# Kernel tuning notes

Hardware: AMD Instinct MI355X
Metric: run time of the kernel (lower is better)

Reference implementation:

```python
import jax, jax.numpy as jnp
import numpy as np

N_GROUPS = 32
N_HEADS = 8
EPS = 1e-5


def group_norm(x, w, b):
    # x: [B, C, T]; GroupNorm32 computes in fp32 then casts back
    B, C, T = x.shape
    xf = x.astype(jnp.float32).reshape(B, N_GROUPS, (C // N_GROUPS) * T)
    mean = xf.mean(axis=-1, keepdims=True)
    var = xf.var(axis=-1, keepdims=True)
    xn = ((xf - mean) * jax.lax.rsqrt(var + EPS)).reshape(B, C, T)
    return (xn * w[None, :, None] + b[None, :, None]).astype(x.dtype)


def attention_block(x, norm_w, norm_b, qkv_w, qkv_b, proj_w, proj_b):
    B, C = x.shape[0], x.shape[1]
    spatial = x.shape[2:]
    xr = x.reshape(B, C, -1)  # [B, C, T]
    T = xr.shape[-1]
    h = group_norm(xr, norm_w, norm_b)
    # 1x1 Conv1d == per-position matmul: [B, 3C, T]
    qkv = jnp.einsum('oc,bct->bot', qkv_w, h) + qkv_b[None, :, None]
    ch = C // N_HEADS  # per-head channels
    q, k, v = jnp.split(qkv, 3, axis=1)
    q = q.reshape(B * N_HEADS, ch, T)
    k = k.reshape(B * N_HEADS, ch, T)
    v = v.reshape(B * N_HEADS, ch, T)
    scale = 1.0 / np.sqrt(ch)
    w = jnp.einsum('bct,bcs->bts', q * scale, k)  # [B*H, T, T]
    w = jax.nn.softmax(w.astype(jnp.float32), axis=-1).astype(w.dtype)
    a = jnp.einsum('bts,bcs->bct', w, v).reshape(B, C, T)
    a = jnp.einsum('oc,bct->bot', proj_w, a) + proj_b[None, :, None]
    return (xr + a).reshape(B, C, *spatial)


def setup_inputs() -> dict:
    key = jax.random.key(0)
    ks = jax.random.split(key, 6)
    B, C, H, W = 16, 512, 32, 32
    return {
        'x': jax.random.normal(ks[0], (B, C, H, W), jnp.float32),
        'norm_w': jnp.ones((C,), jnp.float32),
        'norm_b': jnp.zeros((C,), jnp.float32),
        'qkv_w': jax.random.normal(ks[1], (3 * C, C), jnp.float32) * (1.0 / np.sqrt(C)),
        'qkv_b': jax.random.normal(ks[2], (3 * C,), jnp.float32) * 0.02,
        'proj_w': jax.random.normal(ks[3], (C, C), jnp.float32) * (1.0 / np.sqrt(C)),
        'proj_b': jax.random.normal(ks[4], (C,), jnp.float32) * 0.02,
    }


def reference(x, norm_w, norm_b, qkv_w, qkv_b, proj_w, proj_b):
    return attention_block(x, norm_w, norm_b, qkv_w, qkv_b, proj_w, proj_b)
```

## Files before the change

kernel.cpp:

```cpp
#include <hip/hip_runtime.h>
#include <hip/hip_bf16.h>

#define B_ 16
#define C_ 512
#define T_ 1024
#define G_ 32
#define CPG 16
#define NH 8
#define CH 64
#define EPS 1e-5f

typedef __bf16 bf16x8 __attribute__((ext_vector_type(8)));
typedef __bf16 bf16x4 __attribute__((ext_vector_type(4)));
typedef float f32x4 __attribute__((ext_vector_type(4)));
typedef float f32x16 __attribute__((ext_vector_type(16)));
typedef int i32x4 __attribute__((ext_vector_type(4)));

__device__ __forceinline__ void gload16(const __bf16* g, const __bf16* l) {
    __builtin_amdgcn_global_load_lds(
        (const __attribute__((address_space(1))) unsigned int*)(unsigned long long)(uintptr_t)g,
        (__attribute__((address_space(3))) unsigned int*)(unsigned int)(uintptr_t)l,
        16, 0, 0);
}

__global__ __launch_bounds__(256) void convw_kernel(const float* __restrict__ qw,
                                                    const float* __restrict__ pw,
                                                    __bf16* __restrict__ wqb,
                                                    __bf16* __restrict__ wpb) {
    int idx = (blockIdx.x * 256 + threadIdx.x) * 8;
    const float* src;
    __bf16* dst;
    if (idx < 1536 * 512) { src = qw + idx; dst = wqb + idx; }
    else { src = pw + (idx - 1536 * 512); dst = wpb + (idx - 1536 * 512); }
    float4 a = *(const float4*)src, b = *(const float4*)(src + 4);
    bf16x8 t;
    t[0] = (__bf16)a.x; t[1] = (__bf16)a.y; t[2] = (__bf16)a.z; t[3] = (__bf16)a.w;
    t[4] = (__bf16)b.x; t[5] = (__bf16)b.y; t[6] = (__bf16)b.z; t[7] = (__bf16)b.w;
    *(bf16x8*)dst = t;
}

__global__ __launch_bounds__(256) void gn_kernel(const float* __restrict__ x,
                                                 const float* __restrict__ w,
                                                 const float* __restrict__ bvec,
                                                 __bf16* __restrict__ h_t) {
    const int blk = blockIdx.x;
    const int bb = blk >> 5;
    const int g  = blk & 31;
    const size_t base = ((size_t)bb * C_ + (size_t)g * CPG) * T_;
    const float4* xp = (const float4*)(x + base);
    float4 vals[16];
    float s = 0.f, sq = 0.f;
#pragma unroll
    for (int i = 0; i < 16; ++i) {
        float4 v = xp[threadIdx.x + i * 256];
        vals[i] = v;
        s  += v.x + v.y + v.z + v.w;
        sq += v.x * v.x + v.y * v.y + v.z * v.z + v.w * v.w;
    }
#pragma unroll
    for (int off = 32; off > 0; off >>= 1) {
        s  += __shfl_down(s, off);
        sq += __shfl_down(sq, off);
    }
    __shared__ float red[2][4];
    const int lane = threadIdx.x & 63, wid = threadIdx.x >> 6;
    if (lane == 0) { red[0][wid] = s; red[1][wid] = sq; }
    __syncthreads();
    s  = red[0][0] + red[0][1] + red[0][2] + red[0][3];
    sq = red[1][0] + red[1][1] + red[1][2] + red[1][3];
    const float mean = s * (1.f / 16384.f);
    const float var  = sq * (1.f / 16384.f) - mean * mean;
    const float rstd = rsqrtf(var + EPS);
    float scv[16], shv[16];
#pragma unroll
    for (int i = 0; i < 16; ++i) {
        scv[i] = w[g * CPG + i] * rstd;
        shv[i] = bvec[g * CPG + i] - mean * scv[i];
    }
    __bf16* hb = h_t + ((size_t)bb * T_ + 4 * threadIdx.x) * C_ + g * CPG;
#pragma unroll
    for (int j = 0; j < 4; ++j) {
        bf16x8 t0, t1;
#pragma unroll
        for (int i = 0; i < 8; ++i) {
            float f0 = ((const float*)&vals[i])[j];
            float f1 = ((const float*)&vals[i + 8])[j];
            t0[i] = (__bf16)(f0 * scv[i] + shv[i]);
            t1[i] = (__bf16)(f1 * scv[i + 8] + shv[i + 8]);
        }
        *(bf16x8*)(hb + (size_t)j * C_) = t0;
        *(bf16x8*)(hb + (size_t)j * C_ + 8) = t1;
    }
}

template<int MODE>
__global__ __launch_bounds__(256) void gemm_mfma(const __bf16* __restrict__ Wb,
                                                 const float* __restrict__ bias,
                                                 const __bf16* __restrict__ Bin,
                                                 const float* __restrict__ xres,
                                                 __bf16* __restrict__ qt,
                                                 __bf16* __restrict__ kt,
                                                 __bf16* __restrict__ vb,
                                                 float* __restrict__ outp) {
    __shared__ __align__(16) __bf16 smem[18432];
    __bf16* As = smem;
    __bf16* Bt = smem + 8192;
    const int tid = threadIdx.x, lane = tid & 63, wv = tid >> 6;
    const int wr = wv >> 1, wc = wv & 1, frow = lane & 15, fgrp = lane >> 4;
    const int bz = blockIdx.z, o0 = blockIdx.y << 7, t0 = blockIdx.x << 7;
    const int lrow = lane >> 3, lblk = (lane & 7) ^ (lrow & 7);

    const __bf16* gA = Wb + (size_t)(o0 + wv * 32 + lrow) * 512 + lblk * 8;
    const __bf16* gB = Bin + ((size_t)bz * T_ + t0 + wv * 32 + lrow) * 512 + lblk * 8;
    __bf16* lA = As + wv * 32 * 64;
    __bf16* lB = Bt + wv * 32 * 64;
    const int sb0 = (fgrp ^ (frow & 7)) * 8;
    const int sb1 = ((4 + fgrp) ^ (frow & 7)) * 8;

    f32x4 acc[4][4] = {};
    for (int k0 = 0; k0 < 512; k0 += 64) {
#pragma unroll
        for (int j = 0; j < 4; ++j) {
            gload16(gA + j * 4096 + k0, lA + j * 512);
            gload16(gB + j * 4096 + k0, lB + j * 512);
        }
        __syncthreads();
        bf16x8 af[4][2], bfr[4][2];
#pragma unroll
        for (int m = 0; m < 4; ++m) {
            const __bf16* r = As + (wr * 64 + m * 16 + frow) * 64;
            af[m][0] = *(const bf16x8*)(r + sb0);
            af[m][1] = *(const bf16x8*)(r + sb1);
        }
#pragma unroll
        for (int n = 0; n < 4; ++n) {
            const __bf16* r = Bt + (wc * 64 + n * 16 + frow) * 64;
            bfr[n][0] = *(const bf16x8*)(r + sb0);
            bfr[n][1] = *(const bf16x8*)(r + sb1);
        }
#pragma unroll
        for (int kk = 0; kk < 2; ++kk)
#pragma unroll
            for (int m = 0; m < 4; ++m)
#pragma unroll
                for (int n = 0; n < 4; ++n)
                    acc[m][n] = __builtin_amdgcn_mfma_f32_16x16x32_bf16(af[m][kk], bfr[n][kk], acc[m][n], 0, 0, 0);
        __syncthreads();
    }

    float bias_v[4][4];
#pragma unroll
    for (int m = 0; m < 4; ++m)
#pragma unroll
        for (int r = 0; r < 4; ++r)
            bias_v[m][r] = bias[o0 + wr * 64 + m * 16 + fgrp * 4 + r];

    __bf16* e = smem + wv * 4608;
    if (MODE == 0 && o0 < 1024) {
        const float qsc = (o0 < 512) ? 0.18033688f : 1.0f;
#pragma unroll
        for (int m = 0; m < 4; ++m)
#pragma unroll
            for (int n = 0; n < 4; ++n) {
                bf16x4 v;
#pragma unroll
                for (int r = 0; r < 4; ++r) v[r] = (__bf16)((acc[m][n][r] + bias_v[m][r]) * qsc);
                *(bf16x4*)&e[(n * 16 + frow) * 72 + m * 16 + fgrp * 4] = v;
            }
        __syncthreads();
        __bf16* dst = (o0 < 512) ? qt : kt;
        const int ob = o0 & 511;
#pragma unroll
        for (int p = 0; p < 8; ++p) {
            int row = p * 8 + (lane >> 3), c8 = (lane & 7) * 8;
            *(bf16x8*)(dst + ((size_t)bz * T_ + t0 + wc * 64 + row) * 512 + ob + wr * 64 + c8) =
                *(const bf16x8*)&e[row * 72 + c8];
        }
    } else {
#pragma unroll
        for (int m = 0; m < 4; ++m)
#pragma unroll
            for (int n = 0; n < 4; ++n)
#pragma unroll
                for (int r = 0; r < 4; ++r)
                    e[(m * 16 + fgrp * 4 + r) * 72 + n * 16 + frow] =
                        (__bf16)(acc[m][n][r] + bias_v[m][r]);
        __syncthreads();
        if (MODE == 0) {
            const int ob = o0 - 1024;
#pragma unroll
            for (int p = 0; p < 8; ++p) {
                int row = p * 8 + (lane >> 3), c8 = (lane & 7) * 8;
                *(bf16x8*)(vb + ((size_t)bz * C_ + ob + wr * 64 + row) * T_ + t0 + wc * 64 + c8) =
                    *(const bf16x8*)&e[row * 72 + c8];
            }
        } else {
#pragma unroll
            for (int p = 0; p < 8; ++p) {
                int row = p * 8 + (lane >> 3), c8 = (lane & 7) * 8;
                int o = o0 + wr * 64 + row;
                size_t base = ((size_t)bz * C_ + o) * T_ + t0 + wc * 64 + c8;
                bf16x8 v = *(const bf16x8*)&e[row * 72 + c8];
                float4 x0 = *(const float4*)(xres + base);
                float4 x1 = *(const float4*)(xres + base + 4);
                float4 r0, r1;
                r0.x = x0.x + (float)v[0]; r0.y = x0.y + (float)v[1];
                r0.z = x0.z + (float)v[2]; r0.w = x0.w + (float)v[3];
                r1.x = x1.x + (float)v[4]; r1.y = x1.y + (float)v[5];
                r1.z = x1.z + (float)v[6]; r1.w = x1.w + (float)v[7];
                *(float4*)(outp + base) = r0;
                *(float4*)(outp + base + 4) = r1;
            }
        }
    }
}

__global__ __launch_bounds__(256, 2) void attn32_kernel(const __bf16* __restrict__ qt,
                                                        const __bf16* __restrict__ kt,
                                                        const __bf16* __restrict__ vbuf,
                                                        __bf16* __restrict__ aout) {
    __shared__ __align__(16) __bf16 smem[18432];
    const int tid = threadIdx.x, lane = tid & 63, wv = tid >> 6;
    const int ln = lane & 31, hi = lane >> 5;
    const int lin = blockIdx.x;
    const int work = (lin & 7) * 64 + (lin >> 3);
    const int head = work >> 2;
    const int bb = head >> 3, hh = head & 7;
    const int tq0 = (work & 3) << 8;

    const __bf16* qbase = qt + (size_t)bb * T_ * 512 + hh * CH;
    const __bf16* kbase = kt + (size_t)bb * T_ * 512 + hh * CH;
    const __bf16* vbase = vbuf + ((size_t)bb * C_ + hh * CH) * T_;

    bf16x8 qf[2][4];
#pragma unroll
    for (int sub = 0; sub < 2; ++sub) {
        const __bf16* qr = qbase + (size_t)(tq0 + wv * 64 + sub * 32 + ln) * 512 + hi * 8;
#pragma unroll
        for (int st = 0; st < 4; ++st) qf[sub][st] = *(const bf16x8*)(qr + st * 16);
    }

    const int r8 = lane >> 3, cbs = (lane & 7) ^ (lane >> 3);
    const int rx = ln & 7;

    f32x16 o00 = {}, o01 = {}, o10 = {}, o11 = {};
    float l0 = 0.f, l1 = 0.f;

#pragma unroll
    for (int c = 0; c < 2; ++c) {
        int ch = wv * 2 + c;
        gload16(kbase + (size_t)(ch * 8 + r8) * 512 + cbs * 8, smem + ch * 512);
        gload16(vbase + (size_t)(ch * 8 + r8) * T_ + cbs * 8, smem + 4096 + ch * 512);
    }
    __syncthreads();

#pragma unroll 2
    for (int it = 0; it < 16; ++it) {
        const int cur = it & 1;
        if (it < 15) {
            const int s0n = (it + 1) << 6;
            __bf16* base = smem + (cur ^ 1) * 8192;
#pragma unroll
            for (int c = 0; c < 2; ++c) {
                int ch = wv * 2 + c;
                gload16(kbase + (size_t)(s0n + ch * 8 + r8) * 512 + cbs * 8, base + ch * 512);
                gload16(vbase + (size_t)(ch * 8 + r8) * T_ + s0n + cbs * 8, base + 4096 + ch * 512);
            }
        }
        const __bf16* Kb = smem + cur * 8192;
        const __bf16* Vb = Kb + 4096;

        f32x16 sa00 = {}, sa01 = {}, sa10 = {}, sa11 = {};
        {
            __builtin_amdgcn_s_setprio(1);
#pragma unroll
            for (int st = 0; st < 4; ++st) {
                const int cb = ((hi + 2 * st) ^ rx) << 3;
                bf16x8 k0 = *(const bf16x8*)(Kb + (size_t)ln * 64 + cb);
                bf16x8 k1 = *(const bf16x8*)(Kb + (size_t)(32 + ln) * 64 + cb);
                sa00 = __builtin_amdgcn_mfma_f32_32x32x16_bf16(k0, qf[0][st], sa00, 0, 0, 0);
                sa01 = __builtin_amdgcn_mfma_f32_32x32x16_bf16(k1, qf[0][st], sa01, 0, 0, 0);
                sa10 = __builtin_amdgcn_mfma_f32_32x32x16_bf16(k0, qf[1][st], sa10, 0, 0, 0);
                sa11 = __builtin_amdgcn_mfma_f32_32x32x16_bf16(k1, qf[1][st], sa11, 0, 0, 0);
            }
            __builtin_amdgcn_s_setprio(0);
        }

        float pa = 0.f, pb = 0.f, pc = 0.f, pd = 0.f;
#pragma unroll
        for (int i = 0; i < 16; ++i) { sa00[i] = __builtin_amdgcn_exp2f(sa00[i]); pa += sa00[i]; }
#pragma unroll
        for (int i = 0; i < 16; ++i) { sa01[i] = __builtin_amdgcn_exp2f(sa01[i]); pb += sa01[i]; }
#pragma unroll
        for (int i = 0; i < 16; ++i) { sa10[i] = __builtin_amdgcn_exp2f(sa10[i]); pc += sa10[i]; }
#pragma unroll
        for (int i = 0; i < 16; ++i) { sa11[i] = __builtin_amdgcn_exp2f(sa11[i]); pd += sa11[i]; }
        l0 += pa + pb;
        l1 += pc + pd;

        bf16x8 pfA[4], pfB[4];
#pragma unroll
        for (int sub = 0; sub < 2; ++sub) {
            const f32x16& s_lo = sub ? sa10 : sa00;
            const f32x16& s_hi = sub ? sa11 : sa01;
            unsigned Wd0[8], Wd1[8];
#pragma unroll
            for (int q = 0; q < 8; ++q) {
                unsigned a0 = (unsigned)__builtin_bit_cast(unsigned short, (__bf16)s_lo[2 * q]);
                unsigned a1 = (unsigned)__builtin_bit_cast(unsigned short, (__bf16)s_lo[2 * q + 1]);
                Wd0[q] = a0 | (a1 << 16);
                unsigned b0 = (unsigned)__builtin_bit_cast(unsigned short, (__bf16)s_hi[2 * q]);
                unsigned b1 = (unsigned)__builtin_bit_cast(unsigned short, (__bf16)s_hi[2 * q + 1]);
                Wd1[q] = b0 | (b1 << 16);
            }
            bf16x8* pf = sub ? pfB : pfA;
#pragma unroll
            for (int st = 0; st < 4; ++st) {
                const unsigned* W = (st >> 1) ? Wd1 : Wd0;
                const int hf = (st & 1) * 4;
                auto r02 = __builtin_amdgcn_permlane32_swap((int)W[hf + 0], (int)W[hf + 2], false, false);
                auto r13 = __builtin_amdgcn_permlane32_swap((int)W[hf + 1], (int)W[hf + 3], false, false);
                i32x4 pk;
                pk[0] = r02[0]; pk[1] = r13[0]; pk[2] = r02[1]; pk[3] = r13[1];
                pf[st] = __builtin_bit_cast(bf16x8, pk);
            }
        }

        {
            __builtin_amdgcn_s_setprio(1);
#pragma unroll
            for (int st = 0; st < 4; ++st) {
                const int cb = ((hi + 2 * st) ^ rx) << 3;
                bf16x8 v0 = *(const bf16x8*)(Vb + (size_t)ln * 64 + cb);
                bf16x8 v1 = *(const bf16x8*)(Vb + (size_t)(32 + ln) * 64 + cb);
                o00 = __builtin_amdgcn_mfma_f32_32x32x16_bf16(v0, pfA[st], o00, 0, 0, 0);
                o01 = __builtin_amdgcn_mfma_f32_32x32x16_bf16(v1, pfA[st], o01, 0, 0, 0);
                o10 = __builtin_amdgcn_mfma_f32_32x32x16_bf16(v0, pfB[st], o10, 0, 0, 0);
                o11 = __builtin_amdgcn_mfma_f32_32x32x16_bf16(v1, pfB[st], o11, 0, 0, 0);
            }
            __builtin_amdgcn_s_setprio(0);
        }
        __syncthreads();
    }

    l0 += __shfl_xor(l0, 32);
    l1 += __shfl_xor(l1, 32);
    const float rl0 = 1.f / l0, rl1 = 1.f / l1;
    __bf16* e = smem;
#pragma unroll
    for (int sub = 0; sub < 2; ++sub) {
        const float rl = sub ? rl1 : rl0;
        const int row = wv * 64 + sub * 32 + ln;
#pragma unroll
        for (int ct = 0; ct < 2; ++ct) {
            const f32x16& oc = sub ? (ct ? o11 : o10) : (ct ? o01 : o00);
#pragma unroll
            for (int q = 0; q < 8; ++q) {
                int c0 = ct * 32 + 2 * (q & 1) + 8 * (q >> 1) + 4 * hi;
                unsigned u0 = (unsigned)__builtin_bit_cast(unsigned short, (__bf16)(oc[2 * q] * rl));
                unsigned u1 = (unsigned)__builtin_bit_cast(unsigned short, (__bf16)(oc[2 * q + 1] * rl));
                *(unsigned*)&e[(size_t)row * 72 + c0] = u0 | (u1 << 16);
            }
        }
    }
    __syncthreads();
    {
        const int r = tid;
        __bf16* dst = aout + ((size_t)bb * T_ + tq0 + r) * 512 + hh * CH;
        const __bf16* er = e + (size_t)r * 72;
#pragma unroll
        for (int k = 0; k < 8; ++k)
            *(bf16x8*)(dst + k * 8) = *(const bf16x8*)(er + k * 8);
    }
}

extern "C" void kernel_launch(void* const* d_in, const int* in_sizes, int n_in,
                              void* d_out, int out_size, void* d_ws, size_t ws_size,
                              hipStream_t stream) {
    const float* x      = (const float*)d_in[0];
    const float* norm_w = (const float*)d_in[1];
    const float* norm_b = (const float*)d_in[2];
    const float* qkv_w  = (const float*)d_in[3];
    const float* qkv_b  = (const float*)d_in[4];
    const float* proj_w = (const float*)d_in[5];
    const float* proj_b = (const float*)d_in[6];
    float* out = (float*)d_out;

    __bf16* h_t = (__bf16*)d_ws;
    __bf16* wqb = h_t + (size_t)8388608;
    __bf16* wpb = wqb + 786432;
    __bf16* qt  = wpb + 262144;
    __bf16* kt  = qt + (size_t)8388608;
    __bf16* vb  = kt + (size_t)8388608;
    __bf16* at  = vb + (size_t)8388608;

    convw_kernel<<<512, 256, 0, stream>>>(qkv_w, proj_w, wqb, wpb);
    gn_kernel<<<512, 256, 0, stream>>>(x, norm_w, norm_b, h_t);
    gemm_mfma<0><<<dim3(8, 12, 16), 256, 0, stream>>>(wqb, qkv_b, h_t, nullptr, qt, kt, vb, nullptr);
    attn32_kernel<<<dim3(512), 256, 0, stream>>>(qt, kt, vb, at);
    gemm_mfma<1><<<dim3(8, 4, 16), 256, 0, stream>>>(wpb, proj_b, at, x, nullptr, nullptr, nullptr, out);
}
```

Baseline: 116.6 us.

## Double KV tile per stage to halve barriers and prefetch V fragments early

The attention kernel now stages 128 keys/values per pipeline step instead of 64. It processes the two 64-key halves inside the step, which halves the number of barrier-synchronised iterations. The V fragments are also read from LDS before the softmax exp and packing, so LDS latency overlaps with VALU work. In exchange, LDS use per block rises from about 36KB to 64KB, which may limit occupancy to two blocks per CU, and the extra V registers add pressure.

```diff
diff --git a/kernel.cpp b/kernel.cpp
--- a/kernel.cpp
+++ b/kernel.cpp
@@ -219,7 +219,7 @@
                                                         const __bf16* __restrict__ kt,
                                                         const __bf16* __restrict__ vbuf,
                                                         __bf16* __restrict__ aout) {
-    __shared__ __align__(16) __bf16 smem[18432];
+    __shared__ __align__(16) __bf16 smem[32768];
     const int tid = threadIdx.x, lane = tid & 63, wv = tid >> 6;
     const int ln = lane & 31, hi = lane >> 5;
     const int lin = blockIdx.x;
@@ -247,98 +247,113 @@
     float l0 = 0.f, l1 = 0.f;
 
 #pragma unroll
-    for (int c = 0; c < 2; ++c) {
-        int ch = wv * 2 + c;
-        gload16(kbase + (size_t)(ch * 8 + r8) * 512 + cbs * 8, smem + ch * 512);
-        gload16(vbase + (size_t)(ch * 8 + r8) * T_ + cbs * 8, smem + 4096 + ch * 512);
+    for (int c = 0; c < 4; ++c) {
+        int g = wv * 4 + c;
+        gload16(kbase + (size_t)(g * 8 + r8) * 512 + cbs * 8, smem + g * 512);
+        int half = g >> 3, ch = g & 7;
+        gload16(vbase + (size_t)(ch * 8 + r8) * T_ + half * 64 + cbs * 8,
+                smem + 8192 + half * 4096 + ch * 512);
     }
     __syncthreads();
 
 #pragma unroll 2
-    for (int it = 0; it < 16; ++it) {
+    for (int it = 0; it < 8; ++it) {
         const int cur = it & 1;
-        if (it < 15) {
-            const int s0n = (it + 1) << 6;
-            __bf16* base = smem + (cur ^ 1) * 8192;
-#pragma unroll
-            for (int c = 0; c < 2; ++c) {
-                int ch = wv * 2 + c;
-                gload16(kbase + (size_t)(s0n + ch * 8 + r8) * 512 + cbs * 8, base + ch * 512);
-                gload16(vbase + (size_t)(ch * 8 + r8) * T_ + s0n + cbs * 8, base + 4096 + ch * 512);
-            }
-        }
-        const __bf16* Kb = smem + cur * 8192;
-        const __bf16* Vb = Kb + 4096;
-
-        f32x16 sa00 = {}, sa01 = {}, sa10 = {}, sa11 = {};
-        {
-            __builtin_amdgcn_s_setprio(1);
+        if (it < 7) {
+            const int s0n = (it + 1) << 7;
+            __bf16* base = smem + (cur ^ 1) * 16384;
+#pragma unroll
+            for (int c = 0; c < 4; ++c) {
+                int g = wv * 4 + c;
+                gload16(kbase + (size_t)(s0n + g * 8 + r8) * 512 + cbs * 8, base + g * 512);
+                int half = g >> 3, ch = g & 7;
+                gload16(vbase + (size_t)(ch * 8 + r8) * T_ + s0n + half * 64 + cbs * 8,
+                        base + 8192 + half * 4096 + ch * 512);
+            }
+        }
+        const __bf16* Kb = smem + cur * 16384;
+        const __bf16* Vb = Kb + 8192;
+
+#pragma unroll
+        for (int cA = 0; cA < 2; ++cA) {
+            const __bf16* Kc = Kb + cA * 4096;
+            const __bf16* Vh = Vb + cA * 4096;
+
+            f32x16 sa00 = {}, sa01 = {}, sa10 = {}, sa11 = {};
+            {
+                __builtin_amdgcn_s_setprio(1);
+#pragma unroll
+                for (int st = 0; st < 4; ++st) {
+                    const int cb = ((hi + 2 * st) ^ rx) << 3;
+                    bf16x8 k0 = *(const bf16x8*)(Kc + (size_t)ln * 64 + cb);
+                    bf16x8 k1 = *(const bf16x8*)(Kc + (size_t)(32 + ln) * 64 + cb);
+                    sa00 = __builtin_amdgcn_mfma_f32_32x32x16_bf16(k0, qf[0][st], sa00, 0, 0, 0);
+                    sa01 = __builtin_amdgcn_mfma_f32_32x32x16_bf16(k1, qf[0][st], sa01, 0, 0, 0);
+                    sa10 = __builtin_amdgcn_mfma_f32_32x32x16_bf16(k0, qf[1][st], sa10, 0, 0, 0);
+                    sa11 = __builtin_amdgcn_mfma_f32_32x32x16_bf16(k1, qf[1][st], sa11, 0, 0, 0);
+                }
+                __builtin_amdgcn_s_setprio(0);
+            }
+
+            bf16x8 vf0[4], vf1[4];
 #pragma unroll
             for (int st = 0; st < 4; ++st) {
                 const int cb = ((hi + 2 * st) ^ rx) << 3;
-                bf16x8 k0 = *(const bf16x8*)(Kb + (size_t)ln * 64 + cb);
-                bf16x8 k1 = *(const bf16x8*)(Kb + (size_t)(32 + ln) * 64 + cb);
-                sa00 = __builtin_amdgcn_mfma_f32_32x32x16_bf16(k0, qf[0][st], sa00, 0, 0, 0);
-                sa01 = __builtin_amdgcn_mfma_f32_32x32x16_bf16(k1, qf[0][st], sa01, 0, 0, 0);
-                sa10 = __builtin_amdgcn_mfma_f32_32x32x16_bf16(k0, qf[1][st], sa10, 0, 0, 0);
-                sa11 = __builtin_amdgcn_mfma_f32_32x32x16_bf16(k1, qf[1][st], sa11, 0, 0, 0);
-            }
-            __builtin_amdgcn_s_setprio(0);
-        }
-
-        float pa = 0.f, pb = 0.f, pc = 0.f, pd = 0.f;
-#pragma unroll
-        for (int i = 0; i < 16; ++i) { sa00[i] = __builtin_amdgcn_exp2f(sa00[i]); pa += sa00[i]; }
-#pragma unroll
-        for (int i = 0; i < 16; ++i) { sa01[i] = __builtin_amdgcn_exp2f(sa01[i]); pb += sa01[i]; }
-#pragma unroll
-        for (int i = 0; i < 16; ++i) { sa10[i] = __builtin_amdgcn_exp2f(sa10[i]); pc += sa10[i]; }
-#pragma unroll
-        for (int i = 0; i < 16; ++i) { sa11[i] = __builtin_amdgcn_exp2f(sa11[i]); pd += sa11[i]; }
-        l0 += pa + pb;
-        l1 += pc + pd;
-
-        bf16x8 pfA[4], pfB[4];
-#pragma unroll
-        for (int sub = 0; sub < 2; ++sub) {
-            const f32x16& s_lo = sub ? sa10 : sa00;
-            const f32x16& s_hi = sub ? sa11 : sa01;
-            unsigned Wd0[8], Wd1[8];
-#pragma unroll
-            for (int q = 0; q < 8; ++q) {
-                unsigned a0 = (unsigned)__builtin_bit_cast(unsigned short, (__bf16)s_lo[2 * q]);
-                unsigned a1 = (unsigned)__builtin_bit_cast(unsigned short, (__bf16)s_lo[2 * q + 1]);
-                Wd0[q] = a0 | (a1 << 16);
-                unsigned b0 = (unsigned)__builtin_bit_cast(unsigned short, (__bf16)s_hi[2 * q]);
-                unsigned b1 = (unsigned)__builtin_bit_cast(unsigned short, (__bf16)s_hi[2 * q + 1]);
-                Wd1[q] = b0 | (b1 << 16);
-            }
-            bf16x8* pf = sub ? pfB : pfA;
-#pragma unroll
-            for (int st = 0; st < 4; ++st) {
-                const unsigned* W = (st >> 1) ? Wd1 : Wd0;
-                const int hf = (st & 1) * 4;
-                auto r02 = __builtin_amdgcn_permlane32_swap((int)W[hf + 0], (int)W[hf + 2], false, false);
-                auto r13 = __builtin_amdgcn_permlane32_swap((int)W[hf + 1], (int)W[hf + 3], false, false);
-                i32x4 pk;
-                pk[0] = r02[0]; pk[1] = r13[0]; pk[2] = r02[1]; pk[3] = r13[1];
-                pf[st] = __builtin_bit_cast(bf16x8, pk);
-            }
-        }
-
-        {
-            __builtin_amdgcn_s_setprio(1);
-#pragma unroll
-            for (int st = 0; st < 4; ++st) {
-                const int cb = ((hi + 2 * st) ^ rx) << 3;
-                bf16x8 v0 = *(const bf16x8*)(Vb + (size_t)ln * 64 + cb);
-                bf16x8 v1 = *(const bf16x8*)(Vb + (size_t)(32 + ln) * 64 + cb);
-                o00 = __builtin_amdgcn_mfma_f32_32x32x16_bf16(v0, pfA[st], o00, 0, 0, 0);
-                o01 = __builtin_amdgcn_mfma_f32_32x32x16_bf16(v1, pfA[st], o01, 0, 0, 0);
-                o10 = __builtin_amdgcn_mfma_f32_32x32x16_bf16(v0, pfB[st], o10, 0, 0, 0);
-                o11 = __builtin_amdgcn_mfma_f32_32x32x16_bf16(v1, pfB[st], o11, 0, 0, 0);
-            }
-            __builtin_amdgcn_s_setprio(0);
+                vf0[st] = *(const bf16x8*)(Vh + (size_t)ln * 64 + cb);
+                vf1[st] = *(const bf16x8*)(Vh + (size_t)(32 + ln) * 64 + cb);
+            }
+
+            float pa = 0.f, pb = 0.f, pc = 0.f, pd = 0.f;
+#pragma unroll
+            for (int i = 0; i < 16; ++i) { sa00[i] = __builtin_amdgcn_exp2f(sa00[i]); pa += sa00[i]; }
+#pragma unroll
+            for (int i = 0; i < 16; ++i) { sa01[i] = __builtin_amdgcn_exp2f(sa01[i]); pb += sa01[i]; }
+#pragma unroll
+            for (int i = 0; i < 16; ++i) { sa10[i] = __builtin_amdgcn_exp2f(sa10[i]); pc += sa10[i]; }
+#pragma unroll
+            for (int i = 0; i < 16; ++i) { sa11[i] = __builtin_amdgcn_exp2f(sa11[i]); pd += sa11[i]; }
+            l0 += pa + pb;
+            l1 += pc + pd;
+
+            bf16x8 pfA[4], pfB[4];
+#pragma unroll
+            for (int sub = 0; sub < 2; ++sub) {
+                const f32x16& s_lo = sub ? sa10 : sa00;
+                const f32x16& s_hi = sub ? sa11 : sa01;
+                unsigned Wd0[8], Wd1[8];
+#pragma unroll
+                for (int q = 0; q < 8; ++q) {
+                    unsigned a0 = (unsigned)__builtin_bit_cast(unsigned short, (__bf16)s_lo[2 * q]);
+                    unsigned a1 = (unsigned)__builtin_bit_cast(unsigned short, (__bf16)s_lo[2 * q + 1]);
+                    Wd0[q] = a0 | (a1 << 16);
+                    unsigned b0 = (unsigned)__builtin_bit_cast(unsigned short, (__bf16)s_hi[2 * q]);
+                    unsigned b1 = (unsigned)__builtin_bit_cast(unsigned short, (__bf16)s_hi[2 * q + 1]);
+                    Wd1[q] = b0 | (b1 << 16);
+                }
+                bf16x8* pf = sub ? pfB : pfA;
+#pragma unroll
+                for (int st = 0; st < 4; ++st) {
+                    const unsigned* W = (st >> 1) ? Wd1 : Wd0;
+                    const int hf = (st & 1) * 4;
+                    auto r02 = __builtin_amdgcn_permlane32_swap((int)W[hf + 0], (int)W[hf + 2], false, false);
+                    auto r13 = __builtin_amdgcn_permlane32_swap((int)W[hf + 1], (int)W[hf + 3], false, false);
+                    i32x4 pk;
+                    pk[0] = r02[0]; pk[1] = r13[0]; pk[2] = r02[1]; pk[3] = r13[1];
+                    pf[st] = __builtin_bit_cast(bf16x8, pk);
+                }
+            }
+
+            {
+                __builtin_amdgcn_s_setprio(1);
+#pragma unroll
+                for (int st = 0; st < 4; ++st) {
+                    o00 = __builtin_amdgcn_mfma_f32_32x32x16_bf16(vf0[st], pfA[st], o00, 0, 0, 0);
+                    o01 = __builtin_amdgcn_mfma_f32_32x32x16_bf16(vf1[st], pfA[st], o01, 0, 0, 0);
+                    o10 = __builtin_amdgcn_mfma_f32_32x32x16_bf16(vf0[st], pfB[st], o10, 0, 0, 0);
+                    o11 = __builtin_amdgcn_mfma_f32_32x32x16_bf16(vf1[st], pfB[st], o11, 0, 0, 0);
+                }
+                __builtin_amdgcn_s_setprio(0);
+            }
         }
         __syncthreads();
     }
```

Result: slower. 172.3 us (+47.8%).

## Split attention KV range across two wave groups and merge partial outputs

Applied to the files above, without the earlier changes.

The attention kernel now launches 512 threads per block. Two halves of four waves each process disjoint halves of the key/value sequence, with separate double-buffered LDS regions. At the end, one half writes its fp32 partial accumulators and row sums to LDS and the other half adds them before normalising and storing. This doubles the waves per query tile to expose more parallelism and latency hiding, at the cost of more LDS, an extra merge phase with barriers, and register pressure under the new launch bounds.

```diff
diff --git a/kernel.cpp b/kernel.cpp
--- a/kernel.cpp
+++ b/kernel.cpp
@@ -215,12 +215,13 @@
     }
 }
 
-__global__ __launch_bounds__(256, 2) void attn32_kernel(const __bf16* __restrict__ qt,
+__global__ __launch_bounds__(512, 4) void attn32_kernel(const __bf16* __restrict__ qt,
                                                         const __bf16* __restrict__ kt,
                                                         const __bf16* __restrict__ vbuf,
                                                         __bf16* __restrict__ aout) {
-    __shared__ __align__(16) __bf16 smem[18432];
+    __shared__ __align__(16) __bf16 smem[33792];
     const int tid = threadIdx.x, lane = tid & 63, wv = tid >> 6;
+    const int w4 = wv & 3, half = wv >> 2;
     const int ln = lane & 31, hi = lane >> 5;
     const int lin = blockIdx.x;
     const int work = (lin & 7) * 64 + (lin >> 3);
@@ -235,39 +236,41 @@
     bf16x8 qf[2][4];
 #pragma unroll
     for (int sub = 0; sub < 2; ++sub) {
-        const __bf16* qr = qbase + (size_t)(tq0 + wv * 64 + sub * 32 + ln) * 512 + hi * 8;
+        const __bf16* qr = qbase + (size_t)(tq0 + w4 * 64 + sub * 32 + ln) * 512 + hi * 8;
 #pragma unroll
         for (int st = 0; st < 4; ++st) qf[sub][st] = *(const bf16x8*)(qr + st * 16);
     }
 
     const int r8 = lane >> 3, cbs = (lane & 7) ^ (lane >> 3);
     const int rx = ln & 7;
+    const int sbase = half << 9;
+    __bf16* const hbuf = smem + half * 16384;
 
     f32x16 o00 = {}, o01 = {}, o10 = {}, o11 = {};
     float l0 = 0.f, l1 = 0.f;
 
 #pragma unroll
     for (int c = 0; c < 2; ++c) {
-        int ch = wv * 2 + c;
-        gload16(kbase + (size_t)(ch * 8 + r8) * 512 + cbs * 8, smem + ch * 512);
-        gload16(vbase + (size_t)(ch * 8 + r8) * T_ + cbs * 8, smem + 4096 + ch * 512);
+        int ch = w4 * 2 + c;
+        gload16(kbase + (size_t)(sbase + ch * 8 + r8) * 512 + cbs * 8, hbuf + ch * 512);
+        gload16(vbase + (size_t)(ch * 8 + r8) * T_ + sbase + cbs * 8, hbuf + 4096 + ch * 512);
     }
     __syncthreads();
 
 #pragma unroll 2
-    for (int it = 0; it < 16; ++it) {
+    for (int it = 0; it < 8; ++it) {
         const int cur = it & 1;
-        if (it < 15) {
-            const int s0n = (it + 1) << 6;
-            __bf16* base = smem + (cur ^ 1) * 8192;
+        if (it < 7) {
+            const int s0n = sbase + ((it + 1) << 6);
+            __bf16* base = hbuf + (cur ^ 1) * 8192;
 #pragma unroll
             for (int c = 0; c < 2; ++c) {
-                int ch = wv * 2 + c;
+                int ch = w4 * 2 + c;
                 gload16(kbase + (size_t)(s0n + ch * 8 + r8) * 512 + cbs * 8, base + ch * 512);
                 gload16(vbase + (size_t)(ch * 8 + r8) * T_ + s0n + cbs * 8, base + 4096 + ch * 512);
             }
         }
-        const __bf16* Kb = smem + cur * 8192;
+        const __bf16* Kb = hbuf + cur * 8192;
         const __bf16* Vb = Kb + 4096;
 
         f32x16 sa00 = {}, sa01 = {}, sa10 = {}, sa11 = {};
@@ -345,31 +348,62 @@
 
     l0 += __shfl_xor(l0, 32);
     l1 += __shfl_xor(l1, 32);
-    const float rl0 = 1.f / l0, rl1 = 1.f / l1;
+    float* ex  = (float*)smem;
+    float* lex = (float*)smem + 16384;
+    const int lsw = lane & 15;
+    if (half) {
+#pragma unroll
+        for (int q = 0; q < 16; ++q) {
+            const f32x16& ov = (q < 4) ? o00 : (q < 8) ? o01 : (q < 12) ? o10 : o11;
+            const int b = (q & 3) * 4;
+            float4 t = make_float4(ov[b], ov[b + 1], ov[b + 2], ov[b + 3]);
+            *(float4*)&ex[(size_t)w4 * 4096 + lane * 64 + (q ^ lsw) * 4] = t;
+        }
+        lex[w4 * 128 + lane * 2]     = l0;
+        lex[w4 * 128 + lane * 2 + 1] = l1;
+    }
+    __syncthreads();
+    if (!half) {
+        const float* src = ex + (size_t)w4 * 4096 + lane * 64;
+#pragma unroll
+        for (int q = 0; q < 16; ++q) {
+            float4 t = *(const float4*)&src[(q ^ lsw) * 4];
+            f32x16& ov = (q < 4) ? o00 : (q < 8) ? o01 : (q < 12) ? o10 : o11;
+            const int b = (q & 3) * 4;
+            ov[b] += t.x; ov[b + 1] += t.y; ov[b + 2] += t.z; ov[b + 3] += t.w;
+        }
+        l0 += lex[w4 * 128 + lane * 2];
+        l1 += lex[w4 * 128 + lane * 2 + 1];
+    }
+    __syncthreads();
+
     __bf16* e = smem;
-#pragma unroll
-    for (int sub = 0; sub < 2; ++sub) {
-        const float rl = sub ? rl1 : rl0;
-        const int row = wv * 64 + sub * 32 + ln;
-#pragma unroll
-        for (int ct = 0; ct < 2; ++ct) {
-            const f32x16& oc = sub ? (ct ? o11 : o10) : (ct ? o01 : o00);
-#pragma unroll
-            for (int q = 0; q < 8; ++q) {
-                int c0 = ct * 32 + 2 * (q & 1) + 8 * (q >> 1) + 4 * hi;
-                unsigned u0 = (unsigned)__builtin_bit_cast(unsigned short, (__bf16)(oc[2 * q] * rl));
-                unsigned u1 = (unsigned)__builtin_bit_cast(unsigned short, (__bf16)(oc[2 * q + 1] * rl));
-                *(unsigned*)&e[(size_t)row * 72 + c0] = u0 | (u1 << 16);
+    if (!half) {
+        const float rl0 = 1.f / l0, rl1 = 1.f / l1;
+#pragma unroll
+        for (int sub = 0; sub < 2; ++sub) {
+            const float rl = sub ? rl1 : rl0;
+            const int row = w4 * 64 + sub * 32 + ln;
+#pragma unroll
+            for (int ct = 0; ct < 2; ++ct) {
+                const f32x16& oc = sub ? (ct ? o11 : o10) : (ct ? o01 : o00);
+#pragma unroll
+                for (int q = 0; q < 8; ++q) {
+                    int c0 = ct * 32 + 2 * (q & 1) + 8 * (q >> 1) + 4 * hi;
+                    unsigned u0 = (unsigned)__builtin_bit_cast(unsigned short, (__bf16)(oc[2 * q] * rl));
+                    unsigned u1 = (unsigned)__builtin_bit_cast(unsigned short, (__bf16)(oc[2 * q + 1] * rl));
+                    *(unsigned*)&e[(size_t)row * 72 + c0] = u0 | (u1 << 16);
+                }
             }
         }
     }
     __syncthreads();
     {
-        const int r = tid;
-        __bf16* dst = aout + ((size_t)bb * T_ + tq0 + r) * 512 + hh * CH;
-        const __bf16* er = e + (size_t)r * 72;
-#pragma unroll
-        for (int k = 0; k < 8; ++k)
+        const int r = tid >> 1, ch2 = tid & 1;
+        __bf16* dst = aout + ((size_t)bb * T_ + tq0 + r) * 512 + hh * CH + ch2 * 32;
+        const __bf16* er = e + (size_t)r * 72 + ch2 * 32;
+#pragma unroll
+        for (int k = 0; k < 4; ++k)
             *(bf16x8*)(dst + k * 8) = *(const bf16x8*)(er + k * 8);
     }
 }
@@ -397,6 +431,6 @@
     convw_kernel<<<512, 256, 0, stream>>>(qkv_w, proj_w, wqb, wpb);
     gn_kernel<<<512, 256, 0, stream>>>(x, norm_w, norm_b, h_t);
     gemm_mfma<0><<<dim3(8, 12, 16), 256, 0, stream>>>(wqb, qkv_b, h_t, nullptr, qt, kt, vb, nullptr);
-    attn32_kernel<<<dim3(512), 256, 0, stream>>>(qt, kt, vb, at);
+    attn32_kernel<<<dim3(512), 512, 0, stream>>>(qt, kt, vb, at);
     gemm_mfma<1><<<dim3(8, 4, 16), 256, 0, stream>>>(wpb, proj_b, at, x, nullptr, nullptr, nullptr, out);
 }
```

Result: slower. 412.5 us (+253.9%).
